# Performance work log

Measured on AMD Instinct MI355X. Metric: run time of the kernel, lower is better.

## Reference

```python
import jax, jax.numpy as jnp
import numpy as np


def setup_inputs() -> dict:
    B, M, N, DEG, MAX_ITER = 256, 8192, 16384, 10, 30
    key = jax.random.key(0)
    k1, k2 = jax.random.split(key)
    rng = np.random.default_rng(0)
    cols = rng.integers(0, N, size=(M, DEG))
    cols[::2, -1] = N  # dummy (padding) entries on half the check rows; index N is the dummy column
    V_c_col = jnp.asarray(cols, dtype=jnp.int32)
    V_c_row = jnp.asarray(np.repeat(np.arange(M)[:, None], DEG, axis=1), dtype=jnp.int32)
    synd = jax.random.randint(k1, (B, M), 0, 2).astype(jnp.float32)
    llr0 = jax.random.normal(k2, (B, N), dtype=jnp.float32) + 2.0  # LLRs biased toward 'no error'
    return {"synd": synd, "llr0": llr0, "V_c_row": V_c_row, "V_c_col": V_c_col, "max_iter": MAX_ITER}


def _decode(synd, llr0, V_c_row, V_c_col, max_iter):
    B, M = synd.shape
    N = llr0.shape[1]
    dtype = llr0.dtype
    mask_dummy = (V_c_col == N)            # [M, DEG]
    cols_flat = V_c_col.reshape(-1)        # [M*DEG]
    inf = jnp.asarray(jnp.inf, dtype)
    # extended variable axis: real variables + one dummy column pinned to +inf LLR
    u_init = jnp.concatenate([llr0, jnp.full((B, 1), jnp.inf, dtype)], axis=1)   # [B, N+1]
    synd_neg = jnp.where(synd == 0, 1.0, -1.0).astype(dtype)[:, V_c_row]          # [B, M, DEG]
    message0 = u_init[:, V_c_col]                                                 # [B, M, DEG]
    l_v0 = jnp.zeros((B, N + 1), dtype)
    zeros_bn = jnp.zeros((B, N + 1), dtype)
    init = (message0, l_v0, zeros_bn, zeros_bn,
            jnp.full((B,), -1, jnp.int32), jnp.zeros((B,), jnp.int32))

    def step(carry, i):
        message, l_v, e_out, l_out, num_iters, conv = carry
        # vn_update: first iteration passes initial messages through unchanged
        a = jnp.where(i == 1, message, l_v[:, V_c_col] - message)
        # cn_update: normalized min-sum, beta = 1 - 2^{-i}
        beta = jnp.asarray(1.0, dtype) - jnp.power(jnp.asarray(2.0, dtype), -(i.astype(dtype)))
        sign = jnp.sign(a)
        sign = jnp.where(sign == 0, jnp.asarray(-1.0, dtype), sign)
        q_sign = synd_neg * jnp.prod(sign, axis=2, keepdims=True)
        ab = jnp.abs(a)
        srt = jnp.sort(ab, axis=2)
        min0, min1 = srt[:, :, :1], srt[:, :, 1:2]
        min_res = jnp.where(ab == min0, min1, min0)
        b = beta * sign * q_sign * min_res
        b = jnp.where(mask_dummy[None, :, :], jnp.asarray(0.0, dtype), b)
        # llr_update: scatter-add check->variable messages onto the intrinsic LLRs
        l_v = u_init.at[:, cols_flat].add(b.reshape(B, -1))
        l_v = l_v.at[:, -1].set(inf)
        e_v = (l_v <= 0).astype(dtype)
        # syndrome estimation: parity of the estimated error over each check's support
        s_est = jnp.mod(jnp.sum(e_v[:, V_c_col], axis=2), 2.0).astype(dtype)
        ok = jnp.all(s_est == synd, axis=1) & (num_iters == -1)
        num_iters = jnp.where(ok, i.astype(jnp.int32), num_iters)
        conv = jnp.where(ok, 1, conv)
        e_out = jnp.where(ok[:, None], e_v, e_out)
        l_out = jnp.where(ok[:, None], l_v, l_out)
        return (b, l_v, e_out, l_out, num_iters, conv), None

    (message, l_v, e_out, l_out, num_iters, conv), _ = jax.lax.scan(
        step, init, jnp.arange(1, max_iter + 1))
    # rows that never converged take the final-iteration estimate
    unconv = num_iters == -1
    e_v = (l_v <= 0).astype(dtype)
    e_out = jnp.where(unconv[:, None], e_v, e_out)
    l_out = jnp.where(unconv[:, None], l_v, l_out)
    num_iters = jnp.where(unconv, max_iter, num_iters)
    # drop the dummy column, matching e_out[:, :-1] / l_out[:, :-1]
    return e_out[:, :-1], num_iters, l_out[:, :-1], conv


def reference(synd, llr0, V_c_row, V_c_col, max_iter):
    return _decode(synd, llr0, V_c_row, V_c_col, max_iter)
```

## Files before the change

### kernel.cpp

```cpp
#include <hip/hip_runtime.h>
#include <cmath>
#include <cstdint>
#include <cstddef>

#define BB 256
#define MM 8192
#define NN 16384
#define DEG 10
#define MAX_ITER 30
#define PAR_BLOCKS 64

typedef unsigned char  u8;
typedef unsigned short u16;


__global__ void k_init(int* colcnt, int* colfill, int* mm, int* niter, int* conv, int* cnt) {
    int t = blockIdx.x * blockDim.x + threadIdx.x;
    if (t < NN) { colcnt[t] = 0; colfill[t] = 0; }
    if (t < BB) { mm[t] = 0; niter[t] = -1; conv[t] = 0; }
    if (t == 0) *cnt = 0;
}

__global__ void k_transpose_f32(const float* __restrict__ in, float* __restrict__ out,
                                float* __restrict__ out2, int R, int C) {
    __shared__ float tile[64][65];
    int c0 = blockIdx.x * 64;
    int r0 = blockIdx.y * 64;
    #pragma unroll
    for (int k = 0; k < 16; k++) {
        int idx = k * 256 + threadIdx.x;
        int i = idx >> 6, j = idx & 63;
        tile[i][j] = in[(size_t)(r0 + i) * C + (c0 + j)];
    }
    __syncthreads();
    #pragma unroll
    for (int k = 0; k < 16; k++) {
        int idx = k * 256 + threadIdx.x;
        int i = idx >> 6, j = idx & 63;
        float v = tile[j][i];
        size_t o = (size_t)(c0 + i) * R + (r0 + j);
        out[o] = v;
        if (out2) out2[o] = v;
    }
}

__global__ void k_synd_t(const float* __restrict__ synd, u8* __restrict__ syndb) {
    __shared__ float tile[64][65];
    int c0 = blockIdx.x * 64;
    int r0 = blockIdx.y * 64;
    #pragma unroll
    for (int k = 0; k < 16; k++) {
        int idx = k * 256 + threadIdx.x;
        int i = idx >> 6, j = idx & 63;
        tile[i][j] = synd[(size_t)(r0 + i) * MM + (c0 + j)];
    }
    __syncthreads();
    #pragma unroll
    for (int k = 0; k < 16; k++) {
        int idx = k * 256 + threadIdx.x;
        int i = idx >> 6, j = idx & 63;
        syndb[(size_t)(c0 + i) * BB + (r0 + j)] = (tile[j][i] != 0.0f) ? 1 : 0;
    }
}

__global__ void k_hist(const int* __restrict__ vc, int* colcnt) {
    int e = blockIdx.x * 256 + threadIdx.x;
    if (e >= MM * DEG) return;
    int c = vc[e];
    if (c < NN) atomicAdd(&colcnt[c], 1);
}

__global__ void k_scan(const int* __restrict__ colcnt, int* __restrict__ colptr) {
    __shared__ int part[256];
    __shared__ int base[257];
    int t = threadIdx.x;
    int s = 0;
    for (int i = 0; i < 64; i++) s += colcnt[t * 64 + i];
    part[t] = s;
    __syncthreads();
    if (t == 0) {
        int acc = 0;
        for (int i = 0; i < 256; i++) { base[i] = acc; acc += part[i]; }
        base[256] = acc;
    }
    __syncthreads();
    int acc = base[t];
    for (int i = 0; i < 64; i++) { int c = t * 64 + i; colptr[c] = acc; acc += colcnt[c]; }
    if (t == 255) colptr[NN] = base[256];
}

__global__ void k_fill(const int* __restrict__ vc, const int* __restrict__ colptr,
                       int* colfill, int* coledges) {
    int e = blockIdx.x * 256 + threadIdx.x;
    if (e >= MM * DEG) return;
    int c = vc[e];
    if (c < NN) {
        int p = colptr[c] + atomicAdd(&colfill[c], 1);
        coledges[p] = e;
    }
}

__global__ void k_sort(const int* __restrict__ colptr, int* coledges) {
    int n = blockIdx.x * 256 + threadIdx.x;
    if (n >= NN) return;
    int p0 = colptr[n], p1 = colptr[n + 1];
    for (int i = p0 + 1; i < p1; i++) {
        int v = coledges[i];
        int j = i - 1;
        while (j >= p0 && coledges[j] > v) { coledges[j + 1] = coledges[j]; j--; }
        coledges[j + 1] = v;
    }
}


__global__ void k_check4(const int* __restrict__ vc, const float* __restrict__ lv,
                         float* __restrict__ svv, u16* __restrict__ sbits,
                         const u8* __restrict__ syndb,
                         int* __restrict__ niter, int* __restrict__ conv,
                         int* __restrict__ mm, int* __restrict__ cnt,
                         float beta, int first, int it_prev) {
    __shared__ int cs[4 * DEG];
    __shared__ int s_stop, s_last;
    int bid = blockIdx.x, t = threadIdx.x;

    if (it_prev > 0 && bid < PAR_BLOCKS) {
        bool frozen = (niter[t] != -1);
        volatile int* vmm = (volatile int*)mm;
        for (int m = bid; m < MM; m += PAR_BLOCKS) {
            if (t == 0) s_stop = 1;
            __syncthreads();
            bool flagged = frozen || (vmm[t] != 0);
            if (!flagged) s_stop = 0;
            __syncthreads();
            if (s_stop) break;
            if (!flagged) {
                unsigned par = 0;
                #pragma unroll
                for (int d = 0; d < DEG; d++) {
                    int c = vc[m * DEG + d];
                    if (c < NN) par ^= (lv[(size_t)c * BB + t] <= 0.0f) ? 1u : 0u;
                }
                if (par != (unsigned)syndb[(size_t)m * BB + t]) atomicOr(&mm[t], 1);
            }
        }
        __syncthreads();
        __threadfence();
        if (t == 0) {
            int tk = atomicAdd(cnt, 1);
            s_last = (tk == PAR_BLOCKS - 1) ? 1 : 0;
        }
        __syncthreads();
        if (s_last) {
            int mmv = atomicAdd(&mm[t], 0);
            if (niter[t] == -1 && mmv == 0) { niter[t] = it_prev; conv[t] = 1; }
            mm[t] = 0;
            if (t == 0) *cnt = 0;
            __threadfence();
        }
        __syncthreads();
    }

    if (t < 4 * DEG) cs[t] = vc[bid * 4 * DEG + t];
    __syncthreads();

    int w = t >> 6, l = t & 63;
    int m = bid * 4 + w, b4 = l * 4;
    size_t mb = (size_t)m * BB + b4;

    float pv0[4], pv1[4];
    unsigned pb[4];
    if (!first) {
        float4 q0 = *(const float4*)(svv + mb * 2);
        float4 q1 = *(const float4*)(svv + mb * 2 + 4);
        ushort4 pbv = *(const ushort4*)(sbits + mb);
        pv0[0] = q0.x; pv1[0] = q0.y; pv0[1] = q0.z; pv1[1] = q0.w;
        pv0[2] = q1.x; pv1[2] = q1.y; pv0[3] = q1.z; pv1[3] = q1.w;
        pb[0] = pbv.x; pb[1] = pbv.y; pb[2] = pbv.z; pb[3] = pbv.w;
    } else {
        #pragma unroll
        for (int j = 0; j < 4; j++) { pv0[j] = 0.f; pv1[j] = 0.f; pb[j] = 0; }
    }
    int pi0[4]; unsigned pq[4];
    #pragma unroll
    for (int j = 0; j < 4; j++) { pi0[j] = (pb[j] >> 11) & 15; pq[j] = (pb[j] >> 10) & 1u; }

    float m0[4] = {INFINITY, INFINITY, INFINITY, INFINITY};
    float m1[4] = {INFINITY, INFINITY, INFINITY, INFINITY};
    unsigned neg[4] = {0, 0, 0, 0};
    int i0[4] = {0, 0, 0, 0};

    #pragma unroll
    for (int d = 0; d < DEG; d++) {
        int c = cs[w * DEG + d];
        if (c >= NN) continue;
        float4 g = *(const float4*)(lv + (size_t)c * BB + b4);
        float gj[4] = {g.x, g.y, g.z, g.w};
        #pragma unroll
        for (int j = 0; j < 4; j++) {
            float a;
            if (first) a = gj[j];
            else {
                float tt = (d == pi0[j]) ? pv1[j] : pv0[j];
                unsigned sx = pq[j] ^ ((pb[j] >> d) & 1u);
                a = gj[j] - (sx ? -tt : tt);
            }
            if (!(a > 0.0f)) neg[j] |= 1u << d;
            float x = fabsf(a);
            if (x < m0[j]) { m1[j] = m0[j]; m0[j] = x; i0[j] = d; }
            else if (x < m1[j]) m1[j] = x;
        }
    }

    uchar4 sb = *(const uchar4*)(syndb + mb);
    unsigned sbv[4] = {sb.x, sb.y, sb.z, sb.w};
    unsigned q[4];
    #pragma unroll
    for (int j = 0; j < 4; j++)
        q[j] = (__popc(neg[j]) & 1u) ^ (sbv[j] ? 1u : 0u);

    float v0[4], v1[4];
    #pragma unroll
    for (int j = 0; j < 4; j++) { v0[j] = beta * m0[j]; v1[j] = beta * m1[j]; }

    *(float4*)(svv + mb * 2)     = make_float4(v0[0], v1[0], v0[1], v1[1]);
    *(float4*)(svv + mb * 2 + 4) = make_float4(v0[2], v1[2], v0[3], v1[3]);
    ushort4 nb;
    nb.x = (u16)(neg[0] | (q[0] << 10) | ((unsigned)i0[0] << 11));
    nb.y = (u16)(neg[1] | (q[1] << 10) | ((unsigned)i0[1] << 11));
    nb.z = (u16)(neg[2] | (q[2] << 10) | ((unsigned)i0[2] << 11));
    nb.w = (u16)(neg[3] | (q[3] << 10) | ((unsigned)i0[3] << 11));
    *(ushort4*)(sbits + mb) = nb;
}

__global__ void k_var4(const float* __restrict__ llr0t, const float* __restrict__ svv,
                       const u16* __restrict__ sbits,
                       const int* __restrict__ colptr, const int* __restrict__ coledges,
                       float* __restrict__ lv, const int* __restrict__ niter) {
    int t = threadIdx.x;
    int w = t >> 6, l = t & 63;
    int n = blockIdx.x * 4 + w, b4 = l * 4;

    int4 f = *(const int4*)(niter + b4);
    if (f.x != -1 && f.y != -1 && f.z != -1 && f.w != -1) return;

    float4 s = *(const float4*)(llr0t + (size_t)n * BB + b4);
    int p0 = colptr[n], p1 = colptr[n + 1];
    for (int pp = p0; pp < p1; pp++) {
        int e = coledges[pp];
        int m = e / DEG;
        int d = e - m * DEG;
        size_t mb = (size_t)m * BB + b4;
        float4 q0 = *(const float4*)(svv + mb * 2);
        float4 q1 = *(const float4*)(svv + mb * 2 + 4);
        ushort4 bb = *(const ushort4*)(sbits + mb);
        {
            float tt = (d == ((bb.x >> 11) & 15)) ? q0.y : q0.x;
            unsigned sx = ((bb.x >> 10) ^ (bb.x >> d)) & 1u;
            s.x += sx ? -tt : tt;
        }
        {
            float tt = (d == ((bb.y >> 11) & 15)) ? q0.w : q0.z;
            unsigned sx = ((bb.y >> 10) ^ (bb.y >> d)) & 1u;
            s.y += sx ? -tt : tt;
        }
        {
            float tt = (d == ((bb.z >> 11) & 15)) ? q1.y : q1.x;
            unsigned sx = ((bb.z >> 10) ^ (bb.z >> d)) & 1u;
            s.z += sx ? -tt : tt;
        }
        {
            float tt = (d == ((bb.w >> 11) & 15)) ? q1.w : q1.z;
            unsigned sx = ((bb.w >> 10) ^ (bb.w >> d)) & 1u;
            s.w += sx ? -tt : tt;
        }
    }
    float* dst = lv + (size_t)n * BB + b4;
    if (f.x == -1 && f.y == -1 && f.z == -1 && f.w == -1) {
        *(float4*)dst = s;
    } else {
        if (f.x == -1) dst[0] = s.x;
        if (f.y == -1) dst[1] = s.y;
        if (f.z == -1) dst[2] = s.z;
        if (f.w == -1) dst[3] = s.w;
    }
}

__global__ void k_parity(const int* __restrict__ vc, const float* __restrict__ lv,
                         const u8* __restrict__ syndb, int* __restrict__ niter,
                         int* __restrict__ conv, int* __restrict__ mm,
                         int* __restrict__ cnt, int it) {
    __shared__ int s_stop, s_last;
    int b = threadIdx.x;
    bool frozen = (niter[b] != -1);
    volatile int* vmm = (volatile int*)mm;

    for (int m = blockIdx.x; m < MM; m += PAR_BLOCKS) {
        if (b == 0) s_stop = 1;
        __syncthreads();
        bool flagged = frozen || (vmm[b] != 0);
        if (!flagged) s_stop = 0;
        __syncthreads();
        if (s_stop) break;
        if (!flagged) {
            unsigned par = 0;
            #pragma unroll
            for (int d = 0; d < DEG; d++) {
                int c = vc[m * DEG + d];
                if (c < NN) par ^= (lv[(size_t)c * BB + b] <= 0.0f) ? 1u : 0u;
            }
            if (par != (unsigned)syndb[(size_t)m * BB + b]) atomicOr(&mm[b], 1);
        }
    }
    __syncthreads();
    __threadfence();
    if (b == 0) {
        int tk = atomicAdd(cnt, 1);
        s_last = (tk == PAR_BLOCKS - 1) ? 1 : 0;
    }
    __syncthreads();
    if (s_last) {
        int mmv = atomicAdd(&mm[b], 0);
        if (niter[b] == -1 && mmv == 0) { niter[b] = it; conv[b] = 1; }
        mm[b] = 0;
        if (b == 0) *cnt = 0;
    }
}


__global__ void k_out_e(const float* __restrict__ lv, float* __restrict__ out) {
    __shared__ float tile[64][65];
    int c0 = blockIdx.x * 64;
    int r0 = blockIdx.y * 64;
    #pragma unroll
    for (int k = 0; k < 16; k++) {
        int idx = k * 256 + threadIdx.x;
        int i = idx >> 6, j = idx & 63;
        tile[i][j] = (lv[(size_t)(r0 + i) * BB + (c0 + j)] <= 0.0f) ? 1.0f : 0.0f;
    }
    __syncthreads();
    #pragma unroll
    for (int k = 0; k < 16; k++) {
        int idx = k * 256 + threadIdx.x;
        int i = idx >> 6, j = idx & 63;
        out[(size_t)(c0 + i) * NN + (r0 + j)] = tile[j][i];
    }
}

__global__ void k_out_scalars(const int* __restrict__ niter, const int* __restrict__ conv,
                              float* __restrict__ out_ni, float* __restrict__ out_conv) {
    int b = threadIdx.x;
    int ni = niter[b];
    out_ni[b] = (float)(ni == -1 ? MAX_ITER : ni);
    out_conv[b] = (float)conv[b];
}


extern "C" void kernel_launch(void* const* d_in, const int* in_sizes, int n_in,
                              void* d_out, int out_size, void* d_ws, size_t ws_size,
                              hipStream_t stream) {
    const float* synd = (const float*)d_in[0];
    const float* llr0 = (const float*)d_in[1];
    const int* vcol   = (const int*)d_in[3];
    float* out = (float*)d_out;

    char* ws = (char*)d_ws;
    size_t off = 0;
    auto alloc = [&](size_t bytes) {
        off = (off + 255) & ~(size_t)255;
        size_t o = off; off += bytes; return o;
    };
    float* llr0t  = (float*)(ws + alloc((size_t)NN * BB * 4));
    float* lv     = (float*)(ws + alloc((size_t)NN * BB * 4));
    float* svv    = (float*)(ws + alloc((size_t)MM * BB * 8));
    u16*   sbits  = (u16*)(ws + alloc((size_t)MM * BB * 2));
    u8*   syndb   = (u8*)(ws + alloc((size_t)MM * BB));
    int* coledges = (int*)(ws + alloc((size_t)MM * DEG * 4));
    int* colptr   = (int*)(ws + alloc((size_t)(NN + 1) * 4));
    int* colcnt   = (int*)(ws + alloc((size_t)NN * 4));
    int* colfill  = (int*)(ws + alloc((size_t)NN * 4));
    int* mm       = (int*)(ws + alloc((size_t)BB * 4));
    int* niter    = (int*)(ws + alloc((size_t)BB * 4));
    int* conv     = (int*)(ws + alloc((size_t)BB * 4));
    int* cnt      = (int*)(ws + alloc(256));
    (void)in_sizes; (void)n_in; (void)out_size; (void)ws_size;

    k_init<<<NN / 256, 256, 0, stream>>>(colcnt, colfill, mm, niter, conv, cnt);
    k_transpose_f32<<<dim3(NN / 64, BB / 64), 256, 0, stream>>>(llr0, llr0t, lv, BB, NN);
    k_synd_t<<<dim3(MM / 64, BB / 64), 256, 0, stream>>>(synd, syndb);
    k_hist<<<(MM * DEG + 255) / 256, 256, 0, stream>>>(vcol, colcnt);
    k_scan<<<1, 256, 0, stream>>>(colcnt, colptr);
    k_fill<<<(MM * DEG + 255) / 256, 256, 0, stream>>>(vcol, colptr, colfill, coledges);
    k_sort<<<NN / 256, 256, 0, stream>>>(colptr, coledges);

    for (int i = 1; i <= MAX_ITER; i++) {
        float beta = 1.0f - ldexpf(1.0f, -i);
        k_check4<<<MM / 4, 256, 0, stream>>>(vcol, lv, svv, sbits, syndb,
                                             niter, conv, mm, cnt,
                                             beta, (i == 1) ? 1 : 0, i - 1);
        k_var4<<<NN / 4, 256, 0, stream>>>(llr0t, svv, sbits, colptr, coledges, lv, niter);
    }
    k_parity<<<PAR_BLOCKS, 256, 0, stream>>>(vcol, lv, syndb, niter, conv, mm, cnt, MAX_ITER);

    float* out_e    = out;
    float* out_ni   = out + (size_t)BB * NN;
    float* out_l    = out + (size_t)BB * NN + BB;
    float* out_conv = out + 2 * (size_t)BB * NN + BB;
    k_out_e<<<dim3(BB / 64, NN / 64), 256, 0, stream>>>(lv, out_e);
    k_transpose_f32<<<dim3(BB / 64, NN / 64), 256, 0, stream>>>(lv, out_l, nullptr, NN, BB);
    k_out_scalars<<<1, 256, 0, stream>>>(niter, conv, out_ni, out_conv);
}
```

Before: 2.094 ms.

## Partition batch across XCDs and split convergence check into separate kernel

Blocks of the check and variable kernels are remapped so that consecutive block IDs (which round-robin across the 8 XCDs) each own a fixed 32-wide batch slice across 32 rows/columns, aiming to keep each XCD's working set of lv/svv/sbits in its own L2. The syndrome/convergence check previously fused into the first 64 blocks of k_check4 is moved into a separate k_parity launch after each iteration, removing the serialized early-block work from the check kernel at the cost of an extra launch per iteration. Per-thread accesses become shorter strided segments (32 floats per row) rather than full 256-wide rows, which may reduce coalescing.

```diff
diff --git a/kernel.cpp b/kernel.cpp
--- a/kernel.cpp
+++ b/kernel.cpp
@@ -9,6 +9,8 @@
 #define DEG 10
 #define MAX_ITER 30
 #define PAR_BLOCKS 64
+#define NXCD 8
+#define GRP 32
 
 typedef unsigned char  u8;
 typedef unsigned short u16;
@@ -115,56 +117,17 @@
 
 __global__ void k_check4(const int* __restrict__ vc, const float* __restrict__ lv,
                          float* __restrict__ svv, u16* __restrict__ sbits,
-                         const u8* __restrict__ syndb,
-                         int* __restrict__ niter, int* __restrict__ conv,
-                         int* __restrict__ mm, int* __restrict__ cnt,
-                         float beta, int first, int it_prev) {
-    __shared__ int cs[4 * DEG];
-    __shared__ int s_stop, s_last;
+                         const u8* __restrict__ syndb, float beta, int first) {
+    __shared__ int cs[32 * DEG];
     int bid = blockIdx.x, t = threadIdx.x;
-
-    if (it_prev > 0 && bid < PAR_BLOCKS) {
-        bool frozen = (niter[t] != -1);
-        volatile int* vmm = (volatile int*)mm;
-        for (int m = bid; m < MM; m += PAR_BLOCKS) {
-            if (t == 0) s_stop = 1;
-            __syncthreads();
-            bool flagged = frozen || (vmm[t] != 0);
-            if (!flagged) s_stop = 0;
-            __syncthreads();
-            if (s_stop) break;
-            if (!flagged) {
-                unsigned par = 0;
-                #pragma unroll
-                for (int d = 0; d < DEG; d++) {
-                    int c = vc[m * DEG + d];
-                    if (c < NN) par ^= (lv[(size_t)c * BB + t] <= 0.0f) ? 1u : 0u;
-                }
-                if (par != (unsigned)syndb[(size_t)m * BB + t]) atomicOr(&mm[t], 1);
-            }
-        }
-        __syncthreads();
-        __threadfence();
-        if (t == 0) {
-            int tk = atomicAdd(cnt, 1);
-            s_last = (tk == PAR_BLOCKS - 1) ? 1 : 0;
-        }
-        __syncthreads();
-        if (s_last) {
-            int mmv = atomicAdd(&mm[t], 0);
-            if (niter[t] == -1 && mmv == 0) { niter[t] = it_prev; conv[t] = 1; }
-            mm[t] = 0;
-            if (t == 0) *cnt = 0;
-            __threadfence();
-        }
-        __syncthreads();
-    }
-
-    if (t < 4 * DEG) cs[t] = vc[bid * 4 * DEG + t];
-    __syncthreads();
-
-    int w = t >> 6, l = t & 63;
-    int m = bid * 4 + w, b4 = l * 4;
+    int g = bid & (NXCD - 1);
+    int r0 = (bid >> 3) * 32;
+    for (int i = t; i < 32 * DEG; i += 256) cs[i] = vc[r0 * DEG + i];
+    __syncthreads();
+
+    int row = t >> 3;
+    int m = r0 + row;
+    int b4 = g * GRP + (t & 7) * 4;
     size_t mb = (size_t)m * BB + b4;
 
     float pv0[4], pv1[4];
@@ -191,10 +154,10 @@
 
     #pragma unroll
     for (int d = 0; d < DEG; d++) {
-        int c = cs[w * DEG + d];
+        int c = cs[row * DEG + d];
         if (c >= NN) continue;
-        float4 g = *(const float4*)(lv + (size_t)c * BB + b4);
-        float gj[4] = {g.x, g.y, g.z, g.w};
+        float4 gv = *(const float4*)(lv + (size_t)c * BB + b4);
+        float gj[4] = {gv.x, gv.y, gv.z, gv.w};
         #pragma unroll
         for (int j = 0; j < 4; j++) {
             float a;
@@ -236,9 +199,11 @@
                        const u16* __restrict__ sbits,
                        const int* __restrict__ colptr, const int* __restrict__ coledges,
                        float* __restrict__ lv, const int* __restrict__ niter) {
-    int t = threadIdx.x;
-    int w = t >> 6, l = t & 63;
-    int n = blockIdx.x * 4 + w, b4 = l * 4;
+    int bid = blockIdx.x, t = threadIdx.x;
+    int g = bid & (NXCD - 1);
+    int n0 = (bid >> 3) * 32;
+    int n = n0 + (t >> 3);
+    int b4 = g * GRP + (t & 7) * 4;
 
     int4 f = *(const int4*)(niter + b4);
     if (f.x != -1 && f.y != -1 && f.z != -1 && f.w != -1) return;
@@ -394,12 +359,12 @@
 
     for (int i = 1; i <= MAX_ITER; i++) {
         float beta = 1.0f - ldexpf(1.0f, -i);
-        k_check4<<<MM / 4, 256, 0, stream>>>(vcol, lv, svv, sbits, syndb,
-                                             niter, conv, mm, cnt,
-                                             beta, (i == 1) ? 1 : 0, i - 1);
-        k_var4<<<NN / 4, 256, 0, stream>>>(llr0t, svv, sbits, colptr, coledges, lv, niter);
-    }
-    k_parity<<<PAR_BLOCKS, 256, 0, stream>>>(vcol, lv, syndb, niter, conv, mm, cnt, MAX_ITER);
+        k_check4<<<(MM / 32) * NXCD, 256, 0, stream>>>(vcol, lv, svv, sbits, syndb,
+                                                       beta, (i == 1) ? 1 : 0);
+        k_var4<<<(NN / 32) * NXCD, 256, 0, stream>>>(llr0t, svv, sbits, colptr,
+                                                     coledges, lv, niter);
+        k_parity<<<PAR_BLOCKS, 256, 0, stream>>>(vcol, lv, syndb, niter, conv, mm, cnt, i);
+    }
 
     float* out_e    = out;
     float* out_ni   = out + (size_t)BB * NN;
```

Result: faster. 1.715 ms (-18.1%).
